# Kernel optimization log

Measured on AMD Instinct MI355X. Metric: run time of the kernel, lower is better.

## Reference

```python
import jax, jax.numpy as jnp
import numpy as np

N_SRC = 50000
N_DST = 50000
N_EDGES = 800000
D_IN = 128
D_HID = 128
D_OUT = 128


def setup_inputs() -> dict:
    key = jax.random.key(0)
    ks = jax.random.split(key, 8)
    h_src = jax.random.normal(ks[0], (N_SRC, D_IN), dtype=jnp.float32)
    h_dst = jax.random.normal(ks[1], (N_DST, D_IN), dtype=jnp.float32)
    weights = jax.random.uniform(ks[2], (N_EDGES,), dtype=jnp.float32)
    edge_src = jax.random.randint(ks[3], (N_EDGES,), 0, N_SRC, dtype=jnp.int64)
    edge_dst = jax.random.randint(ks[4], (N_EDGES,), 0, N_DST, dtype=jnp.int64)
    # Xavier-uniform-ish init scaled like nn.init.xavier_uniform_(gain=sqrt(2))
    gain = float(np.sqrt(2.0))
    limQ = gain * float(np.sqrt(6.0 / (D_IN + D_HID)))
    limW = gain * float(np.sqrt(6.0 / (D_IN + D_HID + D_OUT)))
    Q_w = jax.random.uniform(ks[5], (D_HID, D_IN), minval=-limQ, maxval=limQ, dtype=jnp.float32)
    Q_b = jnp.zeros((D_HID,), dtype=jnp.float32)
    W_w = jax.random.uniform(ks[6], (D_OUT, D_IN + D_HID), minval=-limW, maxval=limW, dtype=jnp.float32)
    W_b = jnp.zeros((D_OUT,), dtype=jnp.float32)
    return {
        "h_src": h_src, "h_dst": h_dst, "weights": weights,
        "edge_src": edge_src, "edge_dst": edge_dst,
        "Q_w": Q_w, "Q_b": Q_b, "W_w": W_w, "W_b": W_b,
    }


def reference(h_src, h_dst, weights, edge_src, edge_dst, Q_w, Q_b, W_w, W_b):
    # n = relu(Q(h_src))  (dropout is identity in eval mode)
    n_src = jax.nn.relu(h_src @ Q_w.T + Q_b)                    # [N_src, H]
    w = weights.astype(jnp.float32)
    # u_mul_e + sum: weighted message aggregation per destination node
    msgs = n_src[edge_src] * w[:, None]                          # [E, H]
    n = jax.ops.segment_sum(msgs, edge_dst, num_segments=N_DST)  # [N_dst, H]
    # copy_e + sum: per-destination weight sum, clamped at 1
    ws = jax.ops.segment_sum(w, edge_dst, num_segments=N_DST)
    ws = jnp.clip(ws, 1.0, None)[:, None]                        # [N_dst, 1]
    z_in = jnp.concatenate([n / ws, h_dst], axis=1)              # [N_dst, H+D]
    z = jax.nn.relu(z_in @ W_w.T + W_b)                          # [N_dst, O]
    return z
```

## Files before the change

### kernel.cpp

```cpp
#include <hip/hip_runtime.h>
#include <hip/hip_bf16.h>

#define D 128
#define NBUCK 196
#define CAP 6144
#define P1_EPB 2048
#define QPAD 136
#define WPAD 264

typedef __attribute__((ext_vector_type(8))) short bf16x8;
typedef __attribute__((ext_vector_type(4))) float floatx4;

__device__ __forceinline__ unsigned short f2bf(float f) {
    unsigned u = __float_as_uint(f);
    return (unsigned short)((u + 0x7FFFu + ((u >> 16) & 1u)) >> 16);
}
__device__ __forceinline__ float bf2f(unsigned short s) {
    return __uint_as_float(((unsigned)s) << 16);
}

__global__ __launch_bounds__(256)
void prep(const float* __restrict__ Qw, const float* __restrict__ Ww,
          unsigned short* __restrict__ Qw16, unsigned short* __restrict__ Ww16,
          int* __restrict__ gcursor) {
    int i = blockIdx.x * 256 + threadIdx.x;
    if (i < 256) gcursor[i] = 0;
    if (i < 128 * 128) Qw16[i] = f2bf(Qw[i]);
    if (i < 128 * 256) Ww16[i] = f2bf(Ww[i]);
}

__global__ __launch_bounds__(256)
void gemm1_mfma(const float* __restrict__ h, const unsigned short* __restrict__ Qw,
                const float* __restrict__ Qb, unsigned short* __restrict__ nsrc, int M) {
    __shared__ unsigned short Bs[128 * QPAD];
    const int tid = threadIdx.x;
    const int lane = tid & 63;
    const int wv = tid >> 6;
    const int m0 = (blockIdx.x * 4 + wv) * 16;
    const int rquad = lane >> 4;
    const int rlow = lane & 15;
    const bool active = (m0 < M);

    bf16x8 a[4];
    if (active) {
#pragma unroll
        for (int q = 0; q < 4; ++q) {
            const float* pa = h + (size_t)(m0 + rlow) * D + q * 32 + rquad * 8;
            float4 x = *(const float4*)pa;
            float4 y = *(const float4*)(pa + 4);
            bf16x8 t;
            t[0] = (short)f2bf(x.x); t[1] = (short)f2bf(x.y);
            t[2] = (short)f2bf(x.z); t[3] = (short)f2bf(x.w);
            t[4] = (short)f2bf(y.x); t[5] = (short)f2bf(y.y);
            t[6] = (short)f2bf(y.z); t[7] = (short)f2bf(y.w);
            a[q] = t;
        }
    }

#pragma unroll
    for (int c = tid; c < 2048; c += 256) {
        int row = c >> 4, col = (c & 15) * 8;
        *(bf16x8*)&Bs[row * QPAD + col] = *(const bf16x8*)(Qw + row * 128 + col);
    }
    __syncthreads();
    if (!active) return;

    floatx4 acc[8];
#pragma unroll
    for (int n = 0; n < 8; ++n) acc[n] = (floatx4)0.f;

#pragma unroll
    for (int n = 0; n < 8; ++n) {
#pragma unroll
        for (int q = 0; q < 4; ++q) {
            bf16x8 b = *(const bf16x8*)&Bs[(n * 16 + rlow) * QPAD + q * 32 + rquad * 8];
            acc[n] = __builtin_amdgcn_mfma_f32_16x16x32_bf16(a[q], b, acc[n], 0, 0, 0);
        }
    }

#pragma unroll
    for (int n = 0; n < 8; ++n) {
        int col = n * 16 + rlow;
        float bias = Qb[col];
#pragma unroll
        for (int r = 0; r < 4; ++r) {
            int row = m0 + rquad * 4 + r;
            nsrc[(size_t)row * D + col] = f2bf(fmaxf(acc[n][r] + bias, 0.f));
        }
    }
}

__global__ __launch_bounds__(256)
void pass1_bucket(const int* __restrict__ esrc, const int* __restrict__ edst,
                  const float* __restrict__ w, int* __restrict__ gcursor,
                  unsigned long long* __restrict__ staging, int E) {
    __shared__ int cnt[256];
    __shared__ int base[256];
    const int tid = threadIdx.x;
    const int e0 = blockIdx.x * P1_EPB;
    cnt[tid] = 0;
    __syncthreads();
#pragma unroll
    for (int i = 0; i < P1_EPB; i += 256) {
        int e = e0 + i + tid;
        if (e < E) atomicAdd(&cnt[edst[e] >> 8], 1);
    }
    __syncthreads();
    int c = cnt[tid];
    base[tid] = (c > 0) ? atomicAdd(&gcursor[tid], c) : 0;
    cnt[tid] = 0;
    __syncthreads();
#pragma unroll
    for (int i = 0; i < P1_EPB; i += 256) {
        int e = e0 + i + tid;
        if (e < E) {
            int d = edst[e];
            int b = d >> 8;
            int pos = base[b] + atomicAdd(&cnt[b], 1);
            if (pos < CAP) {
                unsigned long long pk =
                    (unsigned long long)(unsigned)(esrc[e] | ((d & 255) << 16)) |
                    ((unsigned long long)__float_as_uint(w[e]) << 32);
                staging[(size_t)b * CAP + pos] = pk;
            }
        }
    }
}

__global__ __launch_bounds__(256)
void bscan(const int* __restrict__ gcursor, int* __restrict__ bbase) {
    __shared__ int s[256];
    int v = (threadIdx.x < NBUCK) ? gcursor[threadIdx.x] : 0;
    s[threadIdx.x] = v;
    __syncthreads();
#pragma unroll
    for (int off = 1; off < 256; off <<= 1) {
        int t = (threadIdx.x >= off) ? s[threadIdx.x - off] : 0;
        __syncthreads();
        s[threadIdx.x] += t;
        __syncthreads();
    }
    bbase[threadIdx.x] = s[threadIdx.x] - v;
}

__global__ __launch_bounds__(256)
void pass2_fill(const unsigned long long* __restrict__ staging,
                const int* __restrict__ gcursor, const int* __restrict__ bbase,
                int* __restrict__ offs, unsigned long long* __restrict__ csr, int N) {
    __shared__ int cntA[256], sB[256], exC[256];
    const int b = blockIdx.x;
    const int tid = threadIdx.x;
    int cnt = gcursor[b];
    if (cnt > CAP) cnt = CAP;
    const int base = bbase[b];
    const unsigned long long* st = staging + (size_t)b * CAP;

    cntA[tid] = 0;
    __syncthreads();
    for (int i = tid; i < cnt; i += 256)
        atomicAdd(&cntA[(int)((st[i] >> 16) & 255)], 1);
    __syncthreads();

    int v = cntA[tid];
    sB[tid] = v;
    __syncthreads();
#pragma unroll
    for (int off = 1; off < 256; off <<= 1) {
        int t = (tid >= off) ? sB[tid - off] : 0;
        __syncthreads();
        sB[tid] += t;
        __syncthreads();
    }
    exC[tid] = sB[tid] - v;
    cntA[tid] = 0;
    __syncthreads();

    int node = b * 256 + tid;
    if (node <= N) offs[node] = base + exC[tid];

    for (int i = tid; i < cnt; i += 256) {
        unsigned long long pk = st[i];
        int dl = (int)((pk >> 16) & 255);
        int slot = base + exC[dl] + atomicAdd(&cntA[dl], 1);
        csr[slot] = (pk & 0xFFFFull) | (pk & 0xFFFFFFFF00000000ull);
    }
}

__global__ __launch_bounds__(256)
void gather(const unsigned long long* __restrict__ csr, const int* __restrict__ offs,
            const unsigned short* __restrict__ nsrc, unsigned short* __restrict__ nout, int N) {
    int node = __builtin_amdgcn_readfirstlane((int)((blockIdx.x * 256 + threadIdx.x) >> 6));
    int lane = threadIdx.x & 63;
    if (node >= N) return;
    int beg = offs[node], end = offs[node + 1];

    float a0 = 0.f, a1 = 0.f, a2 = 0.f, a3 = 0.f;
    float ws0 = 0.f, ws1 = 0.f;
    const int off2 = lane * 2;

    int i = beg;
    for (; i + 8 <= end; i += 8) {
        unsigned long long p[8];
        unsigned v[8];
        float wt[8];
#pragma unroll
        for (int j = 0; j < 8; ++j) p[j] = csr[i + j];
#pragma unroll
        for (int j = 0; j < 8; ++j) {
            wt[j] = __uint_as_float((unsigned)(p[j] >> 32));
            v[j] = *(const unsigned*)(nsrc + (size_t)(unsigned)p[j] * D + off2);
        }
#pragma unroll
        for (int j = 0; j < 8; j += 2) {
            a0 += bf2f((unsigned short)v[j]) * wt[j];
            a1 += bf2f((unsigned short)(v[j] >> 16)) * wt[j];
            a2 += bf2f((unsigned short)v[j + 1]) * wt[j + 1];
            a3 += bf2f((unsigned short)(v[j + 1] >> 16)) * wt[j + 1];
            ws0 += wt[j]; ws1 += wt[j + 1];
        }
    }
    for (; i + 4 <= end; i += 4) {
        unsigned long long p0 = csr[i + 0], p1 = csr[i + 1];
        unsigned long long p2 = csr[i + 2], p3 = csr[i + 3];
        float w0 = __uint_as_float((unsigned)(p0 >> 32));
        float w1 = __uint_as_float((unsigned)(p1 >> 32));
        float w2 = __uint_as_float((unsigned)(p2 >> 32));
        float w3 = __uint_as_float((unsigned)(p3 >> 32));
        unsigned v0 = *(const unsigned*)(nsrc + (size_t)(unsigned)p0 * D + off2);
        unsigned v1 = *(const unsigned*)(nsrc + (size_t)(unsigned)p1 * D + off2);
        unsigned v2 = *(const unsigned*)(nsrc + (size_t)(unsigned)p2 * D + off2);
        unsigned v3 = *(const unsigned*)(nsrc + (size_t)(unsigned)p3 * D + off2);
        a0 += bf2f((unsigned short)v0) * w0; a1 += bf2f((unsigned short)(v0 >> 16)) * w0;
        a2 += bf2f((unsigned short)v1) * w1; a3 += bf2f((unsigned short)(v1 >> 16)) * w1;
        a0 += bf2f((unsigned short)v2) * w2; a1 += bf2f((unsigned short)(v2 >> 16)) * w2;
        a2 += bf2f((unsigned short)v3) * w3; a3 += bf2f((unsigned short)(v3 >> 16)) * w3;
        ws0 += w0 + w2; ws1 += w1 + w3;
    }
    for (; i < end; ++i) {
        unsigned long long p = csr[i];
        float wt = __uint_as_float((unsigned)(p >> 32));
        unsigned v = *(const unsigned*)(nsrc + (size_t)(unsigned)p * D + off2);
        a0 += bf2f((unsigned short)v) * wt; a1 += bf2f((unsigned short)(v >> 16)) * wt;
        ws0 += wt;
    }

    float inv = 1.f / fmaxf(ws0 + ws1, 1.f);
    unsigned outv = (unsigned)f2bf((a0 + a2) * inv) | ((unsigned)f2bf((a1 + a3) * inv) << 16);
    *(unsigned*)(nout + (size_t)node * D + off2) = outv;
}

__global__ __launch_bounds__(256)
void gemm2_mfma(const unsigned short* __restrict__ nnorm, const float* __restrict__ hdst,
                const unsigned short* __restrict__ Ww, const float* __restrict__ Wb,
                float* __restrict__ out, int M) {
    __shared__ unsigned short Bs[128 * WPAD];
    const int tid = threadIdx.x;
    const int lane = tid & 63;
    const int wv = tid >> 6;
    const int m0 = (blockIdx.x * 4 + wv) * 16;
    const int rquad = lane >> 4;
    const int rlow = lane & 15;
    const bool active = (m0 < M);

    bf16x8 a[8];
    if (active) {
#pragma unroll
        for (int q = 0; q < 4; ++q)
            a[q] = *(const bf16x8*)(nnorm + (size_t)(m0 + rlow) * D + q * 32 + rquad * 8);
#pragma unroll
        for (int q = 4; q < 8; ++q) {
            const float* pa = hdst + (size_t)(m0 + rlow) * D + (q - 4) * 32 + rquad * 8;
            float4 x = *(const float4*)pa;
            float4 y = *(const float4*)(pa + 4);
            bf16x8 t;
            t[0] = (short)f2bf(x.x); t[1] = (short)f2bf(x.y);
            t[2] = (short)f2bf(x.z); t[3] = (short)f2bf(x.w);
            t[4] = (short)f2bf(y.x); t[5] = (short)f2bf(y.y);
            t[6] = (short)f2bf(y.z); t[7] = (short)f2bf(y.w);
            a[q] = t;
        }
    }

#pragma unroll
    for (int c = tid; c < 4096; c += 256) {
        int row = c >> 5, col = (c & 31) * 8;
        *(bf16x8*)&Bs[row * WPAD + col] = *(const bf16x8*)(Ww + row * 256 + col);
    }
    __syncthreads();
    if (!active) return;

    floatx4 acc[8];
#pragma unroll
    for (int n = 0; n < 8; ++n) acc[n] = (floatx4)0.f;

#pragma unroll
    for (int n = 0; n < 8; ++n) {
#pragma unroll
        for (int q = 0; q < 8; ++q) {
            bf16x8 b = *(const bf16x8*)&Bs[(n * 16 + rlow) * WPAD + q * 32 + rquad * 8];
            acc[n] = __builtin_amdgcn_mfma_f32_16x16x32_bf16(a[q], b, acc[n], 0, 0, 0);
        }
    }

#pragma unroll
    for (int n = 0; n < 8; ++n) {
        int col = n * 16 + rlow;
        float bias = Wb[col];
#pragma unroll
        for (int r = 0; r < 4; ++r) {
            int row = m0 + rquad * 4 + r;
            out[(size_t)row * D + col] = fmaxf(acc[n][r] + bias, 0.f);
        }
    }
}

extern "C" void kernel_launch(void* const* d_in, const int* in_sizes, int n_in,
                              void* d_out, int out_size, void* d_ws, size_t ws_size,
                              hipStream_t stream) {
    const float* h_src   = (const float*)d_in[0];
    const float* h_dst   = (const float*)d_in[1];
    const float* weights = (const float*)d_in[2];
    const int*   esrc    = (const int*)d_in[3];
    const int*   edst    = (const int*)d_in[4];
    const float* Q_w     = (const float*)d_in[5];
    const float* Q_b     = (const float*)d_in[6];
    const float* W_w     = (const float*)d_in[7];
    const float* W_b     = (const float*)d_in[8];

    const int N_SRC = in_sizes[0] / D;
    const int N_DST = in_sizes[1] / D;
    const int E     = in_sizes[2];

    char* ws = (char*)d_ws;
    int* gcursor = (int*)(ws + 0);
    int* bbase   = (int*)(ws + 1024);
    int* offs    = (int*)(ws + 2048);
    unsigned short* Qw16 = (unsigned short*)(ws + 204800);
    unsigned short* Ww16 = (unsigned short*)(ws + 237568);
    unsigned long long* csr = (unsigned long long*)(ws + 512000);
    unsigned short* nsrc16  = (unsigned short*)(ws + 512000 + (size_t)E * 8);
    char* tail = ws + 512000 + (size_t)E * 8 + (size_t)N_SRC * D * 2;
    unsigned long long* staging = (unsigned long long*)tail;
    unsigned short* nnorm16     = (unsigned short*)tail;

    float* out = (float*)d_out;

    prep<<<128, 256, 0, stream>>>(Q_w, W_w, Qw16, Ww16, gcursor);

    gemm1_mfma<<<(N_SRC + 63) / 64, 256, 0, stream>>>(h_src, Qw16, Q_b, nsrc16, N_SRC);

    pass1_bucket<<<(E + P1_EPB - 1) / P1_EPB, 256, 0, stream>>>(esrc, edst, weights,
                                                                gcursor, staging, E);
    bscan<<<1, 256, 0, stream>>>(gcursor, bbase);
    pass2_fill<<<NBUCK, 256, 0, stream>>>(staging, gcursor, bbase, offs, csr, N_DST);

    gather<<<(N_DST * 64 + 255) / 256, 256, 0, stream>>>(csr, offs, nsrc16, nnorm16, N_DST);

    gemm2_mfma<<<(N_DST + 63) / 64, 256, 0, stream>>>(nnorm16, h_dst, Ww16, W_b, out, N_DST);
}
```

Before: 191.8 us.

## Drop prep and bucket-scan kernels, use fixed-capacity CSR with begin/end pairs

The separate prep kernel goes away. Weight conversion to bf16 now happens inside each GEMM's shared-memory load, and the cursor reset becomes a memset. The bucket prefix-scan kernel is also removed: each bucket's CSR region starts at a fixed b*CAP offset, and per-node begin/end pairs are stored as int2 so gather needs no neighbour lookup. Pass1 handles twice as many edges per block. Together these cut two kernel launches and a serial scan step, at the cost of a sparser CSR layout, repeated weight conversion in every GEMM block, and staging/CSR no longer sharing workspace.

```diff
diff --git a/kernel.cpp b/kernel.cpp
--- a/kernel.cpp
+++ b/kernel.cpp
@@ -2,9 +2,11 @@
 #include <hip/hip_bf16.h>
 
 #define D 128
+#define BSHIFT 8
+#define BSIZE 256
 #define NBUCK 196
 #define CAP 6144
-#define P1_EPB 2048
+#define P1_EPB 4096
 #define QPAD 136
 #define WPAD 264
 
@@ -20,17 +22,7 @@
 }
 
 __global__ __launch_bounds__(256)
-void prep(const float* __restrict__ Qw, const float* __restrict__ Ww,
-          unsigned short* __restrict__ Qw16, unsigned short* __restrict__ Ww16,
-          int* __restrict__ gcursor) {
-    int i = blockIdx.x * 256 + threadIdx.x;
-    if (i < 256) gcursor[i] = 0;
-    if (i < 128 * 128) Qw16[i] = f2bf(Qw[i]);
-    if (i < 128 * 256) Ww16[i] = f2bf(Ww[i]);
-}
-
-__global__ __launch_bounds__(256)
-void gemm1_mfma(const float* __restrict__ h, const unsigned short* __restrict__ Qw,
+void gemm1_mfma(const float* __restrict__ h, const float* __restrict__ Qw,
                 const float* __restrict__ Qb, unsigned short* __restrict__ nsrc, int M) {
     __shared__ unsigned short Bs[128 * QPAD];
     const int tid = threadIdx.x;
@@ -58,9 +50,12 @@
     }
 
 #pragma unroll
-    for (int c = tid; c < 2048; c += 256) {
-        int row = c >> 4, col = (c & 15) * 8;
-        *(bf16x8*)&Bs[row * QPAD + col] = *(const bf16x8*)(Qw + row * 128 + col);
+    for (int c = tid; c < 4096; c += 256) {
+        int row = c >> 5, col4 = (c & 31) * 4;
+        float4 x = *(const float4*)(Qw + row * 128 + col4);
+        ushort4 t;
+        t.x = f2bf(x.x); t.y = f2bf(x.y); t.z = f2bf(x.z); t.w = f2bf(x.w);
+        *(ushort4*)&Bs[row * QPAD + col4] = t;
     }
     __syncthreads();
     if (!active) return;
@@ -94,32 +89,34 @@
 void pass1_bucket(const int* __restrict__ esrc, const int* __restrict__ edst,
                   const float* __restrict__ w, int* __restrict__ gcursor,
                   unsigned long long* __restrict__ staging, int E) {
-    __shared__ int cnt[256];
-    __shared__ int base[256];
+    __shared__ int cnt[NBUCK];
+    __shared__ int base[NBUCK];
     const int tid = threadIdx.x;
     const int e0 = blockIdx.x * P1_EPB;
-    cnt[tid] = 0;
+    for (int i = tid; i < NBUCK; i += 256) cnt[i] = 0;
     __syncthreads();
 #pragma unroll
     for (int i = 0; i < P1_EPB; i += 256) {
         int e = e0 + i + tid;
-        if (e < E) atomicAdd(&cnt[edst[e] >> 8], 1);
-    }
-    __syncthreads();
-    int c = cnt[tid];
-    base[tid] = (c > 0) ? atomicAdd(&gcursor[tid], c) : 0;
-    cnt[tid] = 0;
+        if (e < E) atomicAdd(&cnt[edst[e] >> BSHIFT], 1);
+    }
+    __syncthreads();
+    for (int i = tid; i < NBUCK; i += 256) {
+        int c = cnt[i];
+        base[i] = (c > 0) ? atomicAdd(&gcursor[i], c) : 0;
+        cnt[i] = 0;
+    }
     __syncthreads();
 #pragma unroll
     for (int i = 0; i < P1_EPB; i += 256) {
         int e = e0 + i + tid;
         if (e < E) {
             int d = edst[e];
-            int b = d >> 8;
+            int b = d >> BSHIFT;
             int pos = base[b] + atomicAdd(&cnt[b], 1);
             if (pos < CAP) {
                 unsigned long long pk =
-                    (unsigned long long)(unsigned)(esrc[e] | ((d & 255) << 16)) |
+                    (unsigned long long)(unsigned)(esrc[e] | ((d & (BSIZE - 1)) << 16)) |
                     ((unsigned long long)__float_as_uint(w[e]) << 32);
                 staging[(size_t)b * CAP + pos] = pk;
             }
@@ -128,31 +125,15 @@
 }
 
 __global__ __launch_bounds__(256)
-void bscan(const int* __restrict__ gcursor, int* __restrict__ bbase) {
-    __shared__ int s[256];
-    int v = (threadIdx.x < NBUCK) ? gcursor[threadIdx.x] : 0;
-    s[threadIdx.x] = v;
-    __syncthreads();
-#pragma unroll
-    for (int off = 1; off < 256; off <<= 1) {
-        int t = (threadIdx.x >= off) ? s[threadIdx.x - off] : 0;
-        __syncthreads();
-        s[threadIdx.x] += t;
-        __syncthreads();
-    }
-    bbase[threadIdx.x] = s[threadIdx.x] - v;
-}
-
-__global__ __launch_bounds__(256)
 void pass2_fill(const unsigned long long* __restrict__ staging,
-                const int* __restrict__ gcursor, const int* __restrict__ bbase,
-                int* __restrict__ offs, unsigned long long* __restrict__ csr, int N) {
+                const int* __restrict__ gcursor,
+                int2* __restrict__ offs2, unsigned long long* __restrict__ csr, int N) {
     __shared__ int cntA[256], sB[256], exC[256];
     const int b = blockIdx.x;
     const int tid = threadIdx.x;
     int cnt = gcursor[b];
     if (cnt > CAP) cnt = CAP;
-    const int base = bbase[b];
+    const int base = b * CAP;
     const unsigned long long* st = staging + (size_t)b * CAP;
 
     cntA[tid] = 0;
@@ -175,8 +156,8 @@
     cntA[tid] = 0;
     __syncthreads();
 
-    int node = b * 256 + tid;
-    if (node <= N) offs[node] = base + exC[tid];
+    int node = b * BSIZE + tid;
+    if (node < N) offs2[node] = make_int2(base + exC[tid], base + exC[tid] + v);
 
     for (int i = tid; i < cnt; i += 256) {
         unsigned long long pk = st[i];
@@ -187,12 +168,13 @@
 }
 
 __global__ __launch_bounds__(256)
-void gather(const unsigned long long* __restrict__ csr, const int* __restrict__ offs,
+void gather(const unsigned long long* __restrict__ csr, const int2* __restrict__ offs2,
             const unsigned short* __restrict__ nsrc, unsigned short* __restrict__ nout, int N) {
     int node = __builtin_amdgcn_readfirstlane((int)((blockIdx.x * 256 + threadIdx.x) >> 6));
     int lane = threadIdx.x & 63;
     if (node >= N) return;
-    int beg = offs[node], end = offs[node + 1];
+    int2 be = offs2[node];
+    int beg = be.x, end = be.y;
 
     float a0 = 0.f, a1 = 0.f, a2 = 0.f, a3 = 0.f;
     float ws0 = 0.f, ws1 = 0.f;
@@ -251,7 +233,7 @@
 
 __global__ __launch_bounds__(256)
 void gemm2_mfma(const unsigned short* __restrict__ nnorm, const float* __restrict__ hdst,
-                const unsigned short* __restrict__ Ww, const float* __restrict__ Wb,
+                const float* __restrict__ Ww, const float* __restrict__ Wb,
                 float* __restrict__ out, int M) {
     __shared__ unsigned short Bs[128 * WPAD];
     const int tid = threadIdx.x;
@@ -282,9 +264,12 @@
     }
 
 #pragma unroll
-    for (int c = tid; c < 4096; c += 256) {
-        int row = c >> 5, col = (c & 31) * 8;
-        *(bf16x8*)&Bs[row * WPAD + col] = *(const bf16x8*)(Ww + row * 256 + col);
+    for (int c = tid; c < 8192; c += 256) {
+        int row = c >> 6, col4 = (c & 63) * 4;
+        float4 x = *(const float4*)(Ww + row * 256 + col4);
+        ushort4 t;
+        t.x = f2bf(x.x); t.y = f2bf(x.y); t.z = f2bf(x.z); t.w = f2bf(x.w);
+        *(ushort4*)&Bs[row * WPAD + col4] = t;
     }
     __syncthreads();
     if (!active) return;
@@ -332,29 +317,26 @@
     const int E     = in_sizes[2];
 
     char* ws = (char*)d_ws;
-    int* gcursor = (int*)(ws + 0);
-    int* bbase   = (int*)(ws + 1024);
-    int* offs    = (int*)(ws + 2048);
-    unsigned short* Qw16 = (unsigned short*)(ws + 204800);
-    unsigned short* Ww16 = (unsigned short*)(ws + 237568);
-    unsigned long long* csr = (unsigned long long*)(ws + 512000);
-    unsigned short* nsrc16  = (unsigned short*)(ws + 512000 + (size_t)E * 8);
-    char* tail = ws + 512000 + (size_t)E * 8 + (size_t)N_SRC * D * 2;
-    unsigned long long* staging = (unsigned long long*)tail;
-    unsigned short* nnorm16     = (unsigned short*)tail;
+    int*  gcursor = (int*)(ws + 0);
+    int2* offs2   = (int2*)(ws + 4096);
+    unsigned long long* staging = (unsigned long long*)(ws + 409600);
+    unsigned long long* csr     = (unsigned long long*)(ws + 409600 + (size_t)NBUCK * CAP * 8);
+    unsigned short* nsrc16  = (unsigned short*)(ws + 409600 + 2 * (size_t)NBUCK * CAP * 8);
+    unsigned short* nnorm16 = (unsigned short*)(ws + 409600 + 2 * (size_t)NBUCK * CAP * 8
+                                                + (size_t)N_SRC * D * 2);
 
     float* out = (float*)d_out;
 
-    prep<<<128, 256, 0, stream>>>(Q_w, W_w, Qw16, Ww16, gcursor);
-
-    gemm1_mfma<<<(N_SRC + 63) / 64, 256, 0, stream>>>(h_src, Qw16, Q_b, nsrc16, N_SRC);
+    hipMemsetAsync(gcursor, 0, NBUCK * sizeof(int), stream);
+
+    gemm1_mfma<<<(N_SRC + 63) / 64, 256, 0, stream>>>(h_src, Q_w, Q_b, nsrc16, N_SRC);
 
     pass1_bucket<<<(E + P1_EPB - 1) / P1_EPB, 256, 0, stream>>>(esrc, edst, weights,
                                                                 gcursor, staging, E);
-    bscan<<<1, 256, 0, stream>>>(gcursor, bbase);
-    pass2_fill<<<NBUCK, 256, 0, stream>>>(staging, gcursor, bbase, offs, csr, N_DST);
-
-    gather<<<(N_DST * 64 + 255) / 256, 256, 0, stream>>>(csr, offs, nsrc16, nnorm16, N_DST);
-
-    gemm2_mfma<<<(N_DST + 63) / 64, 256, 0, stream>>>(nnorm16, h_dst, Ww16, W_b, out, N_DST);
-}
+
+    pass2_fill<<<NBUCK, 256, 0, stream>>>(staging, gcursor, offs2, csr, N_DST);
+
+    gather<<<(N_DST * 64 + 255) / 256, 256, 0, stream>>>(csr, offs2, nsrc16, nnorm16, N_DST);
+
+    gemm2_mfma<<<(N_DST + 63) / 64, 256, 0, stream>>>(nnorm16, h_dst, W_w, W_b, out, N_DST);
+}
```

Result: slower. 197.2 us (+2.8%).
